# Performance work log

Hardware: AMD Instinct MI355X
Metric: run time of the kernel (lower is better)

## Reference

```python
import jax, jax.numpy as jnp
import numpy as np

N_TOKEN = 267735
HEAD = 20000
CUTOFFS = [20000, 20008, 20016, 200000, 267735]  # from cl_root_leaf_dict with 2 roots of 8 leaves
N_ROOTS = 2


def setup_inputs() -> dict:
    key = jax.random.key(0)
    k1, k2, k3, k4 = jax.random.split(key, 4)
    N, D = 1024, 1024
    hidden = jax.random.normal(k1, (N, D), dtype=jnp.float32)
    target = jax.random.randint(k2, (N,), 0, N_TOKEN)
    W = jax.random.normal(k3, (N_TOKEN, D), dtype=jnp.float32) * 0.02
    b = jnp.zeros((N_TOKEN,), dtype=jnp.float32)
    cluster_weight = jax.random.normal(k4, (2, D), dtype=jnp.float32) * 0.02
    cluster_bias = jnp.zeros((2,), dtype=jnp.float32)
    return {"hidden": hidden, "target": target, "W": W, "b": b,
            "cluster_weight": cluster_weight, "cluster_bias": cluster_bias}


def _nll(hidden, target, W, b, cw, cb):
    cutoff_ends = [0] + CUTOFFS
    # head = first 20000 vocab rows + 2 cluster rows (d_proj == d_embed -> no projection)
    head_w = jnp.concatenate([W[:HEAD], cw], axis=0)          # [20002, D]
    head_b = jnp.concatenate([b[:HEAD], cb], axis=0)          # [20002]
    head_lp = jax.nn.log_softmax(hidden @ head_w.T + head_b, axis=-1)  # [N, 20002]
    n_head_cols = head_lp.shape[1]
    rows = jnp.arange(hidden.shape[0])
    # segment 0: target in [0, 20000) -> nll directly from head log-probs
    lp0 = head_lp[rows, jnp.clip(target, 0, HEAD - 1)]
    nll = -lp0  # only valid where target < HEAD; overwritten below otherwise
    for i in range(1, len(CUTOFFS)):
        l, r = cutoff_ends[i], cutoff_ends[i + 1]
        # per-segment tail logits for all tokens (masked combine keeps shapes static)
        tail_lp = jax.nn.log_softmax(hidden @ W[l:r].T + b[l:r], axis=-1)  # [N, r-l]
        # routing column exactly as in the torch code:
        # j = i-1 for root segments, -(i - n_roots) for the two cluster segments
        j = (i - 1) if i <= N_ROOTS else (n_head_cols - (i - N_ROOTS))
        lp_i = head_lp[:, j] + tail_lp[rows, jnp.clip(target - l, 0, r - l - 1)]
        mask = (target >= l) & (target < r)
        nll = jnp.where(mask, -lp_i, nll)
    return nll


def reference(hidden, target, W, b, cluster_weight, cluster_bias):
    return _nll(hidden, target, W, b, cluster_weight, cluster_bias)
```

## Files before the change

kernel.cpp:

```cpp
#include <hip/hip_runtime.h>
#include <hip/hip_bf16.h>

#define D_DIM 1024
#define NTOK 267735
#define NEXT_ 267737
#define HEADN 20000

typedef __attribute__((ext_vector_type(8))) short bf16x8;
typedef __attribute__((ext_vector_type(4))) float f32x4;
typedef __attribute__((ext_vector_type(4))) unsigned uint4v;

__device__ __forceinline__ int seg_of(int c){
  if (c < HEADN)  return 0;
  if (c < 20008)  return 1;
  if (c < 20016)  return 2;
  if (c < 200000) return 3;
  if (c < NTOK)   return 4;
  return 0;
}

__device__ __forceinline__ unsigned pack2(float x, float y){
  __hip_bfloat16 a = __float2bfloat16(x);
  __hip_bfloat16 b = __float2bfloat16(y);
  unsigned short ua = *reinterpret_cast<unsigned short*>(&a);
  unsigned short ub = *reinterpret_cast<unsigned short*>(&b);
  return (unsigned)ua | ((unsigned)ub << 16);
}

#define BM 256
#define BN 128
#define BK 32
#define NTHREADS 512
#define KSTEPS (D_DIM/BK)
#define NCOLT 2092
#define NBLK 8384

#define APRIME_OFF 32768
#define APRIME_BYTES (1024*1024*2)

__device__ __forceinline__ void stage16(const float* g, unsigned short* l){
  __builtin_amdgcn_global_load_lds(
      (const __attribute__((address_space(1))) void*)g,
      (__attribute__((address_space(3))) void*)l, 16, 0, 0);
}

#define CVTPK(d, x, y) asm("v_cvt_pk_bf16_f32 %0, %1, %2" : "=v"(d) : "v"(x), "v"(y))

__global__ void prep_convert(const float* __restrict__ hidden,
                             unsigned short* __restrict__ Ap)
{
  int t = blockIdx.x * blockDim.x + threadIdx.x;
  int r16 = t & 15, kc = (t >> 4) & 127, rb = t >> 11;
  const float4* src = reinterpret_cast<const float4*>(hidden + ((size_t)(rb*16 + r16) * D_DIM + kc*8));
  float4 x = src[0], y = src[1];
  uint4 o;
  o.x = pack2(x.x, x.y); o.y = pack2(x.z, x.w);
  o.z = pack2(y.x, y.y); o.w = pack2(y.z, y.w);
  reinterpret_cast<uint4*>(Ap)[t] = o;
}

__global__ __launch_bounds__(NTHREADS, 1) void gemm_lse_adir(
    const unsigned short* __restrict__ Ap, const float* __restrict__ W,
    const float* __restrict__ bias,   const float* __restrict__ cw,
    const float* __restrict__ cb,     float* __restrict__ accg)
{
  const int b = blockIdx.x;
  const int k8 = b & 7;
  const int sq_ = b >> 3;
  const int xb = sq_ & 3;
  const int yb = (sq_ >> 2) * 8 + k8;
  if (yb >= NCOLT) return;

  __shared__ unsigned short lsB0[BN * 64];
  __shared__ unsigned short lsB1[BN * 64];

  const int tid = threadIdx.x;
  const int rowBase = xb * BM;
  const int colBase = yb * BN;

  const int lane = tid & 63;
  const int wv = tid >> 6;
  const int wm = wv >> 1;
  const int wn = wv & 1;
  const int q  = lane >> 4;
  const int r16 = lane & 15;

  const float* sp;
  {
    int srow = wv*16 + (lane >> 2);
    int c    = (lane & 3) ^ ((srow >> 1) & 3);
    int col  = colBase + srow;
    const float* base = (col < NTOK)  ? (W  + (size_t)col * D_DIM)
                      : (col < NEXT_) ? (cw + (size_t)(col - NTOK) * D_DIM) : W;
    sp = base + c*4;
  }
  const int dstH0 = wv*512;
  const int dstH1 = 4096 + wv*512;

#define STAGE(Lbuf, kn) do{ \
    stage16(sp + (kn)*BK,      &Lbuf[dstH0]); \
    stage16(sp + (kn)*BK + 16, &Lbuf[dstH1]); }while(0)

  int loO[4], hiO[4];
#pragma unroll
  for (int j=0;j<4;++j){
    int row = wn*64 + j*16 + r16;
    int swz = (row >> 1) & 3;
    int h   = q >> 1;
    loO[j] = h*4096 + row*32 + (((2*q  ) & 3) ^ swz)*8;
    hiO[j] = h*4096 + row*32 + (((2*q+1) & 3) ^ swz)*8;
  }

  const unsigned short* a0 = Ap + (size_t)(xb*16 + wm*4 + 0)*16384 + q*128 + r16*8;
  const unsigned short* a1 = Ap + (size_t)(xb*16 + wm*4 + 1)*16384 + q*128 + r16*8;
  const unsigned short* a2 = Ap + (size_t)(xb*16 + wm*4 + 2)*16384 + q*128 + r16*8;
  const unsigned short* a3 = Ap + (size_t)(xb*16 + wm*4 + 3)*16384 + q*128 + r16*8;

  f32x4 acc[4][4];
#pragma unroll
  for (int i=0;i<4;++i)
#pragma unroll
    for (int j=0;j<4;++j) acc[i][j] = (f32x4){0.f,0.f,0.f,0.f};

#define BFRAG(Lr, j, out) { \
    float4 lo = *reinterpret_cast<const float4*>(&Lr[loO[j]]); \
    float4 hi = *reinterpret_cast<const float4*>(&Lr[hiO[j]]); \
    unsigned u0,u1,u2,u3; \
    CVTPK(u0, lo.x, lo.y); CVTPK(u1, lo.z, lo.w); \
    CVTPK(u2, hi.x, hi.y); CVTPK(u3, hi.z, hi.w); \
    uint4v uu; uu.x=u0; uu.y=u1; uu.z=u2; uu.w=u3; \
    out = __builtin_bit_cast(bf16x8, uu); }

  STAGE(lsB0, 0);
  __syncthreads();

  for (int kt = 0; kt < KSTEPS; ++kt){
    unsigned short* Lr = (kt & 1) ? lsB1 : lsB0;
    unsigned short* Lw = (kt & 1) ? lsB0 : lsB1;

    bf16x8 af0 = *reinterpret_cast<const bf16x8*>(a0 + kt*512);
    bf16x8 af1 = *reinterpret_cast<const bf16x8*>(a1 + kt*512);
    bf16x8 af2 = *reinterpret_cast<const bf16x8*>(a2 + kt*512);
    bf16x8 af3 = *reinterpret_cast<const bf16x8*>(a3 + kt*512);

    if (kt + 1 < KSTEPS) STAGE(Lw, kt+1);

    bf16x8 b0, b1, b2, b3;
    BFRAG(Lr, 0, b0); BFRAG(Lr, 1, b1); BFRAG(Lr, 2, b2); BFRAG(Lr, 3, b3);

    acc[0][0] = __builtin_amdgcn_mfma_f32_16x16x32_bf16(af0, b0, acc[0][0], 0,0,0);
    acc[0][1] = __builtin_amdgcn_mfma_f32_16x16x32_bf16(af0, b1, acc[0][1], 0,0,0);
    acc[0][2] = __builtin_amdgcn_mfma_f32_16x16x32_bf16(af0, b2, acc[0][2], 0,0,0);
    acc[0][3] = __builtin_amdgcn_mfma_f32_16x16x32_bf16(af0, b3, acc[0][3], 0,0,0);
    acc[1][0] = __builtin_amdgcn_mfma_f32_16x16x32_bf16(af1, b0, acc[1][0], 0,0,0);
    acc[1][1] = __builtin_amdgcn_mfma_f32_16x16x32_bf16(af1, b1, acc[1][1], 0,0,0);
    acc[1][2] = __builtin_amdgcn_mfma_f32_16x16x32_bf16(af1, b2, acc[1][2], 0,0,0);
    acc[1][3] = __builtin_amdgcn_mfma_f32_16x16x32_bf16(af1, b3, acc[1][3], 0,0,0);
    acc[2][0] = __builtin_amdgcn_mfma_f32_16x16x32_bf16(af2, b0, acc[2][0], 0,0,0);
    acc[2][1] = __builtin_amdgcn_mfma_f32_16x16x32_bf16(af2, b1, acc[2][1], 0,0,0);
    acc[2][2] = __builtin_amdgcn_mfma_f32_16x16x32_bf16(af2, b2, acc[2][2], 0,0,0);
    acc[2][3] = __builtin_amdgcn_mfma_f32_16x16x32_bf16(af2, b3, acc[2][3], 0,0,0);
    acc[3][0] = __builtin_amdgcn_mfma_f32_16x16x32_bf16(af3, b0, acc[3][0], 0,0,0);
    acc[3][1] = __builtin_amdgcn_mfma_f32_16x16x32_bf16(af3, b1, acc[3][1], 0,0,0);
    acc[3][2] = __builtin_amdgcn_mfma_f32_16x16x32_bf16(af3, b2, acc[3][2], 0,0,0);
    acc[3][3] = __builtin_amdgcn_mfma_f32_16x16x32_bf16(af3, b3, acc[3][3], 0,0,0);

    __syncthreads();
  }

  int sq[4]; float bq[4];
#pragma unroll
  for (int f=0; f<4; ++f){
    int c = colBase + wn*64 + f*16 + r16;
    if (c < NTOK)       { sq[f] = seg_of(c); bq[f] = bias[c]; }
    else if (c < NEXT_) { sq[f] = 0;         bq[f] = cb[c - NTOK]; }
    else                { sq[f] = -1;        bq[f] = 0.f; }
  }
  int sfirst = seg_of(colBase);
  int clast  = colBase + BN - 1; if (clast > NEXT_-1) clast = NEXT_-1;
  int slast  = seg_of(clast);
  int smin = sfirst, smax = slast;
  if (slast < sfirst){ smin = 0; smax = 4; }

#pragma unroll
  for (int i=0;i<4;++i){
#pragma unroll
    for (int r=0;r<4;++r){
      float e[4];
#pragma unroll
      for (int f=0;f<4;++f) e[f] = __expf(acc[i][f][r] + bq[f]);
      int rowg = rowBase + wm*64 + i*16 + (lane>>4)*4 + r;
      for (int s2 = smin; s2 <= smax; ++s2){
        float p = 0.f;
#pragma unroll
        for (int f=0;f<4;++f) p += (sq[f]==s2) ? e[f] : 0.f;
#pragma unroll
        for (int off=1; off<16; off<<=1) p += __shfl_xor(p, off, 16);
        if ((lane & 15) == 0 && p != 0.f) atomicAdd(&accg[rowg*8 + s2], p);
      }
    }
  }
}

__global__ __launch_bounds__(256) void finalize_kernel(
    const float* __restrict__ hidden, const int* __restrict__ target,
    const float* __restrict__ W,      const float* __restrict__ bias,
    const float* __restrict__ cw,     const float* __restrict__ cb,
    const float* __restrict__ accg,   float* __restrict__ out)
{
  const int row  = blockIdx.x * 4 + (threadIdx.x >> 6);
  const int lane = threadIdx.x & 63;
  const int t = target[row];

  const float4* h4 = reinterpret_cast<const float4*>(hidden + (size_t)row * D_DIM);
  const float4* w1 = reinterpret_cast<const float4*>(W + (size_t)t * D_DIM);
  int s = 0; const float* jraw = W; float jb = 0.f;
  if (t >= HEADN){
    if      (t < 20008)  { s=1; jraw = W;          jb = bias[0]; }
    else if (t < 20016)  { s=2; jraw = W + D_DIM;  jb = bias[1]; }
    else if (t < 200000) { s=3; jraw = cw + D_DIM; jb = cb[1];   }
    else                 { s=4; jraw = cw;         jb = cb[0];   }
  }
  const float4* w2 = reinterpret_cast<const float4*>(jraw);

  float p1 = 0.f, p2 = 0.f;
#pragma unroll
  for (int j=0;j<4;++j){
    float4 hv = h4[lane + 64*j];
    float4 av = w1[lane + 64*j];
    float4 bv = w2[lane + 64*j];
    p1 += hv.x*av.x + hv.y*av.y + hv.z*av.z + hv.w*av.w;
    p2 += hv.x*bv.x + hv.y*bv.y + hv.z*bv.z + hv.w*bv.w;
  }
#pragma unroll
  for (int off=32; off; off>>=1){
    p1 += __shfl_xor(p1, off, 64);
    p2 += __shfl_xor(p2, off, 64);
  }

  if (lane == 0){
    float lseH = __logf(accg[row*8 + 0]);
    float nll;
    if (t < HEADN){
      nll = -(p1 + bias[t] - lseH);
    } else {
      float lseS = __logf(accg[row*8 + s]);
      nll = -((p2 + jb - lseH) + (p1 + bias[t] - lseS));
    }
    out[row] = nll;
  }
}

extern "C" void kernel_launch(void* const* d_in, const int* in_sizes, int n_in,
                              void* d_out, int out_size, void* d_ws, size_t ws_size,
                              hipStream_t stream)
{
  const float* hidden = (const float*)d_in[0];
  const int*   target = (const int*)  d_in[1];
  const float* W      = (const float*)d_in[2];
  const float* bias   = (const float*)d_in[3];
  const float* cw     = (const float*)d_in[4];
  const float* cb     = (const float*)d_in[5];
  float* out  = (float*)d_out;
  float* accg = (float*)d_ws;
  unsigned short* Ap = (unsigned short*)((char*)d_ws + APRIME_OFF);

  hipMemsetAsync(accg, 0, 1024*8*sizeof(float), stream);

  prep_convert<<<512, 256, 0, stream>>>(hidden, Ap);
  gemm_lse_adir<<<NBLK, NTHREADS, 0, stream>>>(Ap, W, bias, cw, cb, accg);
  finalize_kernel<<<256, 256, 0, stream>>>(hidden, target, W, bias, cw, cb, accg, out);
}
```

Before: 830.7 us.

## Deepen W staging to a 4-slot LDS ring with prefetch distance two

Measured after the change: 1.403 ms. 68.9% more time.

```diff
diff --git a/kernel.cpp b/kernel.cpp
--- a/kernel.cpp
+++ b/kernel.cpp
@@ -71,8 +71,7 @@
   const int yb = (sq_ >> 2) * 8 + k8;
   if (yb >= NCOLT) return;
 
-  __shared__ unsigned short lsB0[BN * 64];
-  __shared__ unsigned short lsB1[BN * 64];
+  __shared__ unsigned short lsB[4 * 8192];
 
   const int tid = threadIdx.x;
   const int rowBase = xb * BM;
@@ -97,9 +96,12 @@
   const int dstH0 = wv*512;
   const int dstH1 = 4096 + wv*512;
 
-#define STAGE(Lbuf, kn) do{ \
-    stage16(sp + (kn)*BK,      &Lbuf[dstH0]); \
-    stage16(sp + (kn)*BK + 16, &Lbuf[dstH1]); }while(0)
+#define STAGE_R(kn) do{ \
+    stage16(sp + (kn)*BK,      &lsB[((kn)&3)*8192 + dstH0]); \
+    stage16(sp + (kn)*BK + 16, &lsB[((kn)&3)*8192 + dstH1]); }while(0)
+
+#define BARRAW() do{ asm volatile("s_waitcnt lgkmcnt(0)" ::: "memory"); \
+                     __builtin_amdgcn_s_barrier(); }while(0)
 
   int loO[4], hiO[4];
 #pragma unroll
@@ -122,31 +124,33 @@
 #pragma unroll
     for (int j=0;j<4;++j) acc[i][j] = (f32x4){0.f,0.f,0.f,0.f};
 
-#define BFRAG(Lr, j, out) { \
-    float4 lo = *reinterpret_cast<const float4*>(&Lr[loO[j]]); \
-    float4 hi = *reinterpret_cast<const float4*>(&Lr[hiO[j]]); \
+#define BFRAG(Lp, j, out) { \
+    float4 lo = *reinterpret_cast<const float4*>(&Lp[loO[j]]); \
+    float4 hi = *reinterpret_cast<const float4*>(&Lp[hiO[j]]); \
     unsigned u0,u1,u2,u3; \
     CVTPK(u0, lo.x, lo.y); CVTPK(u1, lo.z, lo.w); \
     CVTPK(u2, hi.x, hi.y); CVTPK(u3, hi.z, hi.w); \
     uint4v uu; uu.x=u0; uu.y=u1; uu.z=u2; uu.w=u3; \
     out = __builtin_bit_cast(bf16x8, uu); }
 
-  STAGE(lsB0, 0);
+  STAGE_R(0);
+  STAGE_R(1);
   __syncthreads();
 
+#pragma unroll 4
   for (int kt = 0; kt < KSTEPS; ++kt){
-    unsigned short* Lr = (kt & 1) ? lsB1 : lsB0;
-    unsigned short* Lw = (kt & 1) ? lsB0 : lsB1;
+    const unsigned short* Lp = lsB + (kt & 3)*8192;
 
     bf16x8 af0 = *reinterpret_cast<const bf16x8*>(a0 + kt*512);
     bf16x8 af1 = *reinterpret_cast<const bf16x8*>(a1 + kt*512);
     bf16x8 af2 = *reinterpret_cast<const bf16x8*>(a2 + kt*512);
     bf16x8 af3 = *reinterpret_cast<const bf16x8*>(a3 + kt*512);
-
-    if (kt + 1 < KSTEPS) STAGE(Lw, kt+1);
+    __builtin_amdgcn_sched_barrier(0);
+
+    if (kt + 2 < KSTEPS) STAGE_R(kt+2);
 
     bf16x8 b0, b1, b2, b3;
-    BFRAG(Lr, 0, b0); BFRAG(Lr, 1, b1); BFRAG(Lr, 2, b2); BFRAG(Lr, 3, b3);
+    BFRAG(Lp, 0, b0); BFRAG(Lp, 1, b1); BFRAG(Lp, 2, b2); BFRAG(Lp, 3, b3);
 
     acc[0][0] = __builtin_amdgcn_mfma_f32_16x16x32_bf16(af0, b0, acc[0][0], 0,0,0);
     acc[0][1] = __builtin_amdgcn_mfma_f32_16x16x32_bf16(af0, b1, acc[0][1], 0,0,0);
@@ -165,7 +169,7 @@
     acc[3][2] = __builtin_amdgcn_mfma_f32_16x16x32_bf16(af3, b2, acc[3][2], 0,0,0);
     acc[3][3] = __builtin_amdgcn_mfma_f32_16x16x32_bf16(af3, b3, acc[3][3], 0,0,0);
 
-    __syncthreads();
+    BARRAW();
   }
 
   int sq[4]; float bq[4];
@@ -191,12 +195,12 @@
       for (int f=0;f<4;++f) e[f] = __expf(acc[i][f][r] + bq[f]);
       int rowg = rowBase + wm*64 + i*16 + (lane>>4)*4 + r;
       for (int s2 = smin; s2 <= smax; ++s2){
-        float p = 0.f;
-#pragma unroll
-        for (int f=0;f<4;++f) p += (sq[f]==s2) ? e[f] : 0.f;
-#pragma unroll
-        for (int off=1; off<16; off<<=1) p += __shfl_xor(p, off, 16);
-        if ((lane & 15) == 0 && p != 0.f) atomicAdd(&accg[rowg*8 + s2], p);
+        float p2 = 0.f;
+#pragma unroll
+        for (int f=0;f<4;++f) p2 += (sq[f]==s2) ? e[f] : 0.f;
+#pragma unroll
+        for (int off=1; off<16; off<<=1) p2 += __shfl_xor(p2, off, 16);
+        if ((lane & 15) == 0 && p2 != 0.f) atomicAdd(&accg[rowg*8 + s2], p2);
       }
     }
   }
```
